# Performance work log

Hardware: AMD Instinct MI355X
Metric: run time of the kernel (lower is better)

Reference implementation:

```python
import jax, jax.numpy as jnp
import numpy as np

N = 8192          # number of samples (atoms)
D_IN = 256        # in_features (descriptor dim)
D_OUT = 256       # out_features
NUM_TYPE = 64     # number of atom types
INIT_VAL = 0.01


def setup_inputs() -> dict:
    key = jax.random.key(0)
    k1, k2, k3, k4 = jax.random.split(key, 4)
    batch_i = jax.random.randint(k1, (N,), 0, NUM_TYPE)                     # [N] type index per sample
    batch_descriptor = jax.random.normal(k2, (N, D_IN), dtype=jnp.float32)  # [N, D_IN]
    layer1 = INIT_VAL * jax.random.normal(k3, (NUM_TYPE, D_OUT, D_IN), dtype=jnp.float32)
    W = INIT_VAL * jax.random.normal(k4, (D_OUT, D_IN), dtype=jnp.float32)  # linear_adjust.weight
    b = jnp.zeros((D_OUT,), dtype=jnp.float32)                              # linear_adjust.bias (init 0)
    return {"batch_i": batch_i, "batch_descriptor": batch_descriptor,
            "layer1": layer1, "W": W, "b": b}


def reference(batch_i, batch_descriptor, layer1, W, b):
    # Per-sample type-indexed weight gather + batched mat-vec (torch.bmm)
    # layer1[batch_i]: [N, D_OUT, D_IN]; descriptor: [N, D_IN] -> [N, D_OUT]
    gathered = layer1[batch_i]
    out = jnp.einsum('noi,ni->no', gathered, batch_descriptor)
    out = jnp.tanh(out)  # ACT assumed tanh (undefined in snippet)
    # linear_adjust: x @ W.T + b
    adjust = batch_descriptor @ W.T + b
    return out + adjust
```

## Files before the change

kernel.cpp:

```cpp
#include <hip/hip_runtime.h>
#include <cstddef>

#define NUM_TYPE 64
#define DD 256
#define NN 8192
#define GM64 192
#define PSTR 264

typedef __bf16 bf16x8 __attribute__((ext_vector_type(8)));
typedef __bf16 bf16x4 __attribute__((ext_vector_type(4)));
typedef float f32x4 __attribute__((ext_vector_type(4)));

__device__ __forceinline__ bf16x4 cvt4(float4 v) {
  bf16x4 h;
  h[0] = (__bf16)v.x; h[1] = (__bf16)v.y; h[2] = (__bf16)v.z; h[3] = (__bf16)v.w;
  return h;
}

__device__ __forceinline__ float tanh_fast(float x) {
  float xc = fminf(fmaxf(x, -15.f), 15.f);
  float e = __expf(2.f * xc);
  return (e - 1.f) / (e + 1.f);
}

__global__ __launch_bounds__(1024) void perm_conv(
    const int* __restrict__ bi,
    const float* __restrict__ desc,
    const float* __restrict__ W,
    int* __restrict__ type_off, int* __restrict__ perm,
    int* __restrict__ gtype, int* __restrict__ gfirst,
    __bf16* __restrict__ descB, __bf16* __restrict__ Wb) {
  const int b = blockIdx.x;
  const int tid = threadIdx.x;
  if (b == 0) {
    __shared__ int wcnt[16][NUM_TYPE];
    __shared__ int wbase[16][NUM_TYPE];
    __shared__ int cnt[NUM_TYPE];
    __shared__ int tstart[NUM_TYPE];
    __shared__ int gbase[NUM_TYPE];
    __shared__ int totals[2];
    const int w = tid >> 6;
    for (int i = tid; i < 16 * NUM_TYPE; i += 1024) ((int*)wcnt)[i] = 0;
    __syncthreads();
    int myv[8];
#pragma unroll
    for (int rnd = 0; rnd < 8; ++rnd) {
      int v = bi[rnd * 1024 + tid];
      myv[rnd] = v;
      atomicAdd(&wcnt[w][v], 1);
    }
    __syncthreads();
    if (tid < NUM_TYPE) {
      int s = 0;
#pragma unroll
      for (int ww = 0; ww < 16; ++ww) { wbase[ww][tid] = s; s += wcnt[ww][tid]; }
      cnt[tid] = s;
    }
    __syncthreads();
    if (tid == 0) {
      int s = 0, p = 0;
      for (int t = 0; t < NUM_TYPE; ++t) {
        tstart[t] = s; gbase[t] = p;
        s += cnt[t];
        p += (cnt[t] + 63) >> 6;
      }
      totals[0] = s; totals[1] = p;
    }
    __syncthreads();
    if (tid < NUM_TYPE) {
      const int c = cnt[tid];
      const int ngr = (c + 63) >> 6;
      const int g0 = gbase[tid];
      const int s0 = tstart[tid];
      for (int j = 0; j < ngr; ++j) { gtype[g0 + j] = tid; gfirst[g0 + j] = s0 + j * 64; }
      type_off[tid] = s0;
#pragma unroll
      for (int ww = 0; ww < 16; ++ww) wbase[ww][tid] += s0;
    }
    if (tid == 0) type_off[NUM_TYPE] = totals[0];
    for (int g = totals[1] + tid; g < GM64; g += 1024) gtype[g] = -1;
    __syncthreads();
#pragma unroll
    for (int rnd = 0; rnd < 8; ++rnd) {
      int v = myv[rnd];
      int p = atomicAdd(&wbase[w][v], 1);
      perm[p] = rnd * 1024 + tid;
    }
  } else {
    const float4* srcD = reinterpret_cast<const float4*>(desc);
    const float4* srcW = reinterpret_cast<const float4*>(W);
#pragma unroll
    for (int it = 0; it < 4; ++it) {
      const int idx = (b - 1) * 4096 + it * 1024 + tid;
      if (idx < 524288)
        *reinterpret_cast<bf16x4*>(descB + (size_t)idx * 4) = cvt4(srcD[idx]);
      else
        *reinterpret_cast<bf16x4*>(Wb + (size_t)(idx - 524288) * 4) = cvt4(srcW[idx - 524288]);
    }
  }
}

__global__ __launch_bounds__(1024, 1) void gemm_resident(
    const __bf16* __restrict__ descB,
    const float* __restrict__ layer1,
    const __bf16* __restrict__ Wb,
    const float* __restrict__ bias,
    const int* __restrict__ type_off,
    const int* __restrict__ perm,
    float* __restrict__ out) {
  extern __shared__ __bf16 lds[];
  __bf16* At = lds;
  __bf16* Ll = lds + 64 * PSTR;
  __bf16* Wl = lds + 2 * 64 * PSTR;

  const int bid = blockIdx.x;
  const int t = bid >> 2;
  const int cb = bid & 3;
  const int off = type_off[t];
  const int limit = type_off[t + 1];
  const int cnt = limit - off;
  if (cnt <= 0) return;
  const int ngr = (cnt + 63) >> 6;

  const int tid = threadIdx.x;
  const int wid = tid >> 6;
  const int lane = tid & 63;
  const int l15 = lane & 15;
  const int lg = lane >> 4;
  const int wr = wid & 3;
  const int wc = wid >> 2;

  {
    const float* Lsrc = layer1 + ((size_t)t * DD + cb * 64) * DD;
#pragma unroll
    for (int it = 0; it < 4; ++it) {
      const int idx = it * 1024 + tid;
      const int col = idx >> 6, seg = idx & 63;
      float4 v = *reinterpret_cast<const float4*>(Lsrc + (size_t)col * DD + seg * 4);
      *reinterpret_cast<bf16x4*>(Ll + col * PSTR + seg * 4) = cvt4(v);
    }
    const __bf16* Wsrc = Wb + (size_t)cb * 64 * DD;
#pragma unroll
    for (int it = 0; it < 2; ++it) {
      const int idx = it * 1024 + tid;
      const int col = idx >> 5, seg = idx & 31;
      *reinterpret_cast<bf16x8*>(Wl + col * PSTR + seg * 8) =
          *reinterpret_cast<const bf16x8*>(Wsrc + (size_t)col * DD + seg * 8);
    }
  }

  const int colg = cb * 64 + wc * 16 + l15;
  const float bv = bias[colg];

  for (int j = 0; j < ngr; ++j) {
    const int first = off + j * 64;
#pragma unroll
    for (int it = 0; it < 2; ++it) {
      const int idx = it * 1024 + tid;
      const int row = idx >> 5, seg = idx & 31;
      const int rr = first + row;
      const int s = (rr < limit) ? perm[rr] : -1;
      bf16x8 v = {};
      if (s >= 0) v = *reinterpret_cast<const bf16x8*>(descB + (size_t)s * DD + seg * 8);
      *reinterpret_cast<bf16x8*>(At + row * PSTR + seg * 8) = v;
    }
    __syncthreads();

    f32x4 accL = {0.f, 0.f, 0.f, 0.f};
    f32x4 accW = {0.f, 0.f, 0.f, 0.f};
#pragma unroll
    for (int kc = 0; kc < 8; ++kc) {
      bf16x8 af = *reinterpret_cast<const bf16x8*>(At + (wr * 16 + l15) * PSTR + kc * 32 + lg * 8);
      bf16x8 bl = *reinterpret_cast<const bf16x8*>(Ll + (wc * 16 + l15) * PSTR + kc * 32 + lg * 8);
      bf16x8 bw = *reinterpret_cast<const bf16x8*>(Wl + (wc * 16 + l15) * PSTR + kc * 32 + lg * 8);
      accL = __builtin_amdgcn_mfma_f32_16x16x32_bf16(af, bl, accL, 0, 0, 0);
      accW = __builtin_amdgcn_mfma_f32_16x16x32_bf16(af, bw, accW, 0, 0, 0);
    }

    const int orow = first + wr * 16 + l15;
    const int sOut = (orow < limit) ? perm[orow] : -1;
#pragma unroll
    for (int i = 0; i < 4; ++i) {
      const int sv = __shfl(sOut, lg * 4 + i, 64);
      if (sv >= 0)
        __builtin_nontemporal_store(tanh_fast(accL[i]) + accW[i] + bv,
                                    out + (size_t)sv * DD + colg);
    }
    __syncthreads();
  }
}

extern "C" void kernel_launch(void* const* d_in, const int* in_sizes, int n_in,
                              void* d_out, int out_size, void* d_ws, size_t ws_size,
                              hipStream_t stream) {
  const int* bi       = (const int*)d_in[0];
  const float* desc   = (const float*)d_in[1];
  const float* layer1 = (const float*)d_in[2];
  const float* W      = (const float*)d_in[3];
  const float* bias   = (const float*)d_in[4];
  float* out = (float*)d_out;

  char* ws = (char*)d_ws;
  int* type_off = (int*)(ws);
  int* gtype    = (int*)(ws + 1024);
  int* gfirst   = (int*)(ws + 4096);
  int* perm     = (int*)(ws + 8192);
  __bf16* descB = (__bf16*)(ws + 65536);
  __bf16* Wb    = (__bf16*)(ws + 65536 + 4194304);

  const int ldsBytes = 3 * 64 * PSTR * 2;

  hipLaunchKernelGGL(perm_conv, dim3(133), dim3(1024), 0, stream,
                     bi, desc, W, type_off, perm, gtype, gfirst, descB, Wb);
  hipLaunchKernelGGL(gemm_resident, dim3(256), dim3(1024), ldsBytes, stream,
                     descB, layer1, Wb, bias, type_off, perm, out);
}
```

Before: 29.08 us.

## Fuse type bucketing and bf16 conversion into single per-type GEMM kernel

Removes the separate permutation/conversion kernel. Each block now scans the full type-index array itself, builds its own row list for its type in LDS with a wave prefix scan, and converts the fp32 descriptor and W to bf16 on load inside the GEMM. This drops one kernel launch and the global round trip of the bf16 copies and the permutation array. In exchange, every block redundantly reads all 8192 type indices, and the descriptor gather now reads fp32 rather than bf16.

Result: slower. 52.11 us (+79.2%).

```diff
diff --git a/kernel.cpp b/kernel.cpp
--- a/kernel.cpp
+++ b/kernel.cpp
@@ -4,7 +4,6 @@
 #define NUM_TYPE 64
 #define DD 256
 #define NN 8192
-#define GM64 192
 #define PSTR 264
 
 typedef __bf16 bf16x8 __attribute__((ext_vector_type(8)));
@@ -23,146 +22,92 @@
   return (e - 1.f) / (e + 1.f);
 }
 
-__global__ __launch_bounds__(1024) void perm_conv(
+__global__ __launch_bounds__(1024, 1) void fused_all(
     const int* __restrict__ bi,
     const float* __restrict__ desc,
+    const float* __restrict__ layer1,
     const float* __restrict__ W,
-    int* __restrict__ type_off, int* __restrict__ perm,
-    int* __restrict__ gtype, int* __restrict__ gfirst,
-    __bf16* __restrict__ descB, __bf16* __restrict__ Wb) {
-  const int b = blockIdx.x;
-  const int tid = threadIdx.x;
-  if (b == 0) {
-    __shared__ int wcnt[16][NUM_TYPE];
-    __shared__ int wbase[16][NUM_TYPE];
-    __shared__ int cnt[NUM_TYPE];
-    __shared__ int tstart[NUM_TYPE];
-    __shared__ int gbase[NUM_TYPE];
-    __shared__ int totals[2];
-    const int w = tid >> 6;
-    for (int i = tid; i < 16 * NUM_TYPE; i += 1024) ((int*)wcnt)[i] = 0;
-    __syncthreads();
-    int myv[8];
-#pragma unroll
-    for (int rnd = 0; rnd < 8; ++rnd) {
-      int v = bi[rnd * 1024 + tid];
-      myv[rnd] = v;
-      atomicAdd(&wcnt[w][v], 1);
-    }
-    __syncthreads();
-    if (tid < NUM_TYPE) {
-      int s = 0;
-#pragma unroll
-      for (int ww = 0; ww < 16; ++ww) { wbase[ww][tid] = s; s += wcnt[ww][tid]; }
-      cnt[tid] = s;
-    }
-    __syncthreads();
-    if (tid == 0) {
-      int s = 0, p = 0;
-      for (int t = 0; t < NUM_TYPE; ++t) {
-        tstart[t] = s; gbase[t] = p;
-        s += cnt[t];
-        p += (cnt[t] + 63) >> 6;
-      }
-      totals[0] = s; totals[1] = p;
-    }
-    __syncthreads();
-    if (tid < NUM_TYPE) {
-      const int c = cnt[tid];
-      const int ngr = (c + 63) >> 6;
-      const int g0 = gbase[tid];
-      const int s0 = tstart[tid];
-      for (int j = 0; j < ngr; ++j) { gtype[g0 + j] = tid; gfirst[g0 + j] = s0 + j * 64; }
-      type_off[tid] = s0;
-#pragma unroll
-      for (int ww = 0; ww < 16; ++ww) wbase[ww][tid] += s0;
-    }
-    if (tid == 0) type_off[NUM_TYPE] = totals[0];
-    for (int g = totals[1] + tid; g < GM64; g += 1024) gtype[g] = -1;
-    __syncthreads();
-#pragma unroll
-    for (int rnd = 0; rnd < 8; ++rnd) {
-      int v = myv[rnd];
-      int p = atomicAdd(&wbase[w][v], 1);
-      perm[p] = rnd * 1024 + tid;
-    }
-  } else {
-    const float4* srcD = reinterpret_cast<const float4*>(desc);
-    const float4* srcW = reinterpret_cast<const float4*>(W);
-#pragma unroll
-    for (int it = 0; it < 4; ++it) {
-      const int idx = (b - 1) * 4096 + it * 1024 + tid;
-      if (idx < 524288)
-        *reinterpret_cast<bf16x4*>(descB + (size_t)idx * 4) = cvt4(srcD[idx]);
-      else
-        *reinterpret_cast<bf16x4*>(Wb + (size_t)(idx - 524288) * 4) = cvt4(srcW[idx - 524288]);
-    }
-  }
-}
-
-__global__ __launch_bounds__(1024, 1) void gemm_resident(
-    const __bf16* __restrict__ descB,
-    const float* __restrict__ layer1,
-    const __bf16* __restrict__ Wb,
     const float* __restrict__ bias,
-    const int* __restrict__ type_off,
-    const int* __restrict__ perm,
     float* __restrict__ out) {
-  extern __shared__ __bf16 lds[];
-  __bf16* At = lds;
-  __bf16* Ll = lds + 64 * PSTR;
-  __bf16* Wl = lds + 2 * 64 * PSTR;
+  extern __shared__ char smem[];
+  __bf16* At = (__bf16*)smem;
+  __bf16* Ll = At + 64 * PSTR;
+  __bf16* Wl = Ll + 64 * PSTR;
+  int* rlist = (int*)(Wl + 64 * PSTR);
+  __shared__ int scanbuf[16];
+  __shared__ int totcnt;
 
   const int bid = blockIdx.x;
   const int t = bid >> 2;
   const int cb = bid & 3;
-  const int off = type_off[t];
-  const int limit = type_off[t + 1];
-  const int cnt = limit - off;
-  if (cnt <= 0) return;
-  const int ngr = (cnt + 63) >> 6;
+  const int tid = threadIdx.x;
+  const int lane = tid & 63;
+  const int wid = tid >> 6;
 
-  const int tid = threadIdx.x;
-  const int wid = tid >> 6;
-  const int lane = tid & 63;
+  int flags = 0, c = 0;
+  const int ebase = tid * 8;
+#pragma unroll
+  for (int k = 0; k < 8; ++k) {
+    const int m = (bi[ebase + k] == t) ? 1 : 0;
+    flags |= m << k;
+    c += m;
+  }
+  int sc = c;
+#pragma unroll
+  for (int d = 1; d < 64; d <<= 1) {
+    const int o = __shfl_up(sc, d, 64);
+    if (lane >= d) sc += o;
+  }
+  if (lane == 63) scanbuf[wid] = sc;
+  __syncthreads();
+  if (tid == 0) {
+    int s = 0;
+#pragma unroll
+    for (int i = 0; i < 16; ++i) { const int v = scanbuf[i]; scanbuf[i] = s; s += v; }
+    totcnt = s;
+  }
+  __syncthreads();
+  int pos = scanbuf[wid] + sc - c;
+#pragma unroll
+  for (int k = 0; k < 8; ++k)
+    if (flags & (1 << k)) rlist[pos++] = ebase + k;
+  const int cnt = totcnt;
+  __syncthreads();
+  if (cnt == 0) return;
+
+  {
+    const float* Lsrc = layer1 + ((size_t)t * DD + cb * 64) * DD;
+    const float* Wsrc = W + (size_t)(cb * 64) * DD;
+#pragma unroll
+    for (int it = 0; it < 4; ++it) {
+      const int idx = it * 1024 + tid;
+      const int col = idx >> 6, seg = idx & 63;
+      *reinterpret_cast<bf16x4*>(Ll + col * PSTR + seg * 4) =
+          cvt4(*reinterpret_cast<const float4*>(Lsrc + (size_t)col * DD + seg * 4));
+      *reinterpret_cast<bf16x4*>(Wl + col * PSTR + seg * 4) =
+          cvt4(*reinterpret_cast<const float4*>(Wsrc + (size_t)col * DD + seg * 4));
+    }
+  }
+
   const int l15 = lane & 15;
   const int lg = lane >> 4;
   const int wr = wid & 3;
   const int wc = wid >> 2;
+  const int colg = cb * 64 + wc * 16 + l15;
+  const float bv = bias[colg];
+  const int ngr = (cnt + 63) >> 6;
 
-  {
-    const float* Lsrc = layer1 + ((size_t)t * DD + cb * 64) * DD;
+  for (int j = 0; j < ngr; ++j) {
+    const int first = j * 64;
+    __syncthreads();
 #pragma unroll
     for (int it = 0; it < 4; ++it) {
       const int idx = it * 1024 + tid;
-      const int col = idx >> 6, seg = idx & 63;
-      float4 v = *reinterpret_cast<const float4*>(Lsrc + (size_t)col * DD + seg * 4);
-      *reinterpret_cast<bf16x4*>(Ll + col * PSTR + seg * 4) = cvt4(v);
-    }
-    const __bf16* Wsrc = Wb + (size_t)cb * 64 * DD;
-#pragma unroll
-    for (int it = 0; it < 2; ++it) {
-      const int idx = it * 1024 + tid;
-      const int col = idx >> 5, seg = idx & 31;
-      *reinterpret_cast<bf16x8*>(Wl + col * PSTR + seg * 8) =
-          *reinterpret_cast<const bf16x8*>(Wsrc + (size_t)col * DD + seg * 8);
-    }
-  }
-
-  const int colg = cb * 64 + wc * 16 + l15;
-  const float bv = bias[colg];
-
-  for (int j = 0; j < ngr; ++j) {
-    const int first = off + j * 64;
-#pragma unroll
-    for (int it = 0; it < 2; ++it) {
-      const int idx = it * 1024 + tid;
-      const int row = idx >> 5, seg = idx & 31;
+      const int row = idx >> 6, seg = idx & 63;
       const int rr = first + row;
-      const int s = (rr < limit) ? perm[rr] : -1;
-      bf16x8 v = {};
-      if (s >= 0) v = *reinterpret_cast<const bf16x8*>(descB + (size_t)s * DD + seg * 8);
-      *reinterpret_cast<bf16x8*>(At + row * PSTR + seg * 8) = v;
+      float4 v = make_float4(0.f, 0.f, 0.f, 0.f);
+      if (rr < cnt) v = *reinterpret_cast<const float4*>(desc + (size_t)rlist[rr] * DD + seg * 4);
+      *reinterpret_cast<bf16x4*>(At + row * PSTR + seg * 4) = cvt4(v);
     }
     __syncthreads();
 
@@ -178,7 +123,7 @@
     }
 
     const int orow = first + wr * 16 + l15;
-    const int sOut = (orow < limit) ? perm[orow] : -1;
+    const int sOut = (orow < cnt) ? rlist[orow] : -1;
 #pragma unroll
     for (int i = 0; i < 4; ++i) {
       const int sv = __shfl(sOut, lg * 4 + i, 64);
@@ -186,7 +131,6 @@
         __builtin_nontemporal_store(tanh_fast(accL[i]) + accW[i] + bv,
                                     out + (size_t)sv * DD + colg);
     }
-    __syncthreads();
   }
 }
 
@@ -200,18 +144,8 @@
   const float* bias   = (const float*)d_in[4];
   float* out = (float*)d_out;
 
-  char* ws = (char*)d_ws;
-  int* type_off = (int*)(ws);
-  int* gtype    = (int*)(ws + 1024);
-  int* gfirst   = (int*)(ws + 4096);
-  int* perm     = (int*)(ws + 8192);
-  __bf16* descB = (__bf16*)(ws + 65536);
-  __bf16* Wb    = (__bf16*)(ws + 65536 + 4194304);
+  const int ldsBytes = 3 * 64 * PSTR * 2 + NN * 4;
 
-  const int ldsBytes = 3 * 64 * PSTR * 2;
-
-  hipLaunchKernelGGL(perm_conv, dim3(133), dim3(1024), 0, stream,
-                     bi, desc, W, type_off, perm, gtype, gfirst, descB, Wb);
-  hipLaunchKernelGGL(gemm_resident, dim3(256), dim3(1024), ldsBytes, stream,
-                     descB, layer1, Wb, bias, type_off, perm, out);
+  hipLaunchKernelGGL(fused_all, dim3(256), dim3(1024), ldsBytes, stream,
+                     bi, desc, layer1, W, bias, out);
 }
```

## Split GEMM into 32-column blocks of 512 threads with type-interleaved grid

Applied to the files above, without the earlier changes.

The resident GEMM now uses 512 blocks of 512 threads, each covering 32 output columns instead of 64. The block index is remapped so neighbouring blocks handle different types, and two blocks can share a CU. The conversion kernel uses twice as many blocks, each doing half the work, and the unused group-table outputs are removed. The barrier moves to the top of the row-group loop. The aim is more parallelism and better load balance across CUs, at the cost of loading the A tile twice per type.

Measured after the change: 25.65 us. -11.8%, faster.

```diff
diff --git a/kernel.cpp b/kernel.cpp
--- a/kernel.cpp
+++ b/kernel.cpp
@@ -28,7 +28,6 @@
     const float* __restrict__ desc,
     const float* __restrict__ W,
     int* __restrict__ type_off, int* __restrict__ perm,
-    int* __restrict__ gtype, int* __restrict__ gfirst,
     __bf16* __restrict__ descB, __bf16* __restrict__ Wb) {
   const int b = blockIdx.x;
   const int tid = threadIdx.x;
@@ -37,8 +36,7 @@
     __shared__ int wbase[16][NUM_TYPE];
     __shared__ int cnt[NUM_TYPE];
     __shared__ int tstart[NUM_TYPE];
-    __shared__ int gbase[NUM_TYPE];
-    __shared__ int totals[2];
+    __shared__ int totals[1];
     const int w = tid >> 6;
     for (int i = tid; i < 16 * NUM_TYPE; i += 1024) ((int*)wcnt)[i] = 0;
     __syncthreads();
@@ -58,27 +56,18 @@
     }
     __syncthreads();
     if (tid == 0) {
-      int s = 0, p = 0;
-      for (int t = 0; t < NUM_TYPE; ++t) {
-        tstart[t] = s; gbase[t] = p;
-        s += cnt[t];
-        p += (cnt[t] + 63) >> 6;
-      }
-      totals[0] = s; totals[1] = p;
+      int s = 0;
+      for (int t = 0; t < NUM_TYPE; ++t) { tstart[t] = s; s += cnt[t]; }
+      totals[0] = s;
     }
     __syncthreads();
     if (tid < NUM_TYPE) {
-      const int c = cnt[tid];
-      const int ngr = (c + 63) >> 6;
-      const int g0 = gbase[tid];
       const int s0 = tstart[tid];
-      for (int j = 0; j < ngr; ++j) { gtype[g0 + j] = tid; gfirst[g0 + j] = s0 + j * 64; }
       type_off[tid] = s0;
 #pragma unroll
       for (int ww = 0; ww < 16; ++ww) wbase[ww][tid] += s0;
     }
     if (tid == 0) type_off[NUM_TYPE] = totals[0];
-    for (int g = totals[1] + tid; g < GM64; g += 1024) gtype[g] = -1;
     __syncthreads();
 #pragma unroll
     for (int rnd = 0; rnd < 8; ++rnd) {
@@ -90,8 +79,8 @@
     const float4* srcD = reinterpret_cast<const float4*>(desc);
     const float4* srcW = reinterpret_cast<const float4*>(W);
 #pragma unroll
-    for (int it = 0; it < 4; ++it) {
-      const int idx = (b - 1) * 4096 + it * 1024 + tid;
+    for (int it = 0; it < 2; ++it) {
+      const int idx = (b - 1) * 2048 + it * 1024 + tid;
       if (idx < 524288)
         *reinterpret_cast<bf16x4*>(descB + (size_t)idx * 4) = cvt4(srcD[idx]);
       else
@@ -100,7 +89,7 @@
   }
 }
 
-__global__ __launch_bounds__(1024, 1) void gemm_resident(
+__global__ __launch_bounds__(512, 2) void gemm_res32(
     const __bf16* __restrict__ descB,
     const float* __restrict__ layer1,
     const __bf16* __restrict__ Wb,
@@ -111,11 +100,11 @@
   extern __shared__ __bf16 lds[];
   __bf16* At = lds;
   __bf16* Ll = lds + 64 * PSTR;
-  __bf16* Wl = lds + 2 * 64 * PSTR;
-
-  const int bid = blockIdx.x;
-  const int t = bid >> 2;
-  const int cb = bid & 3;
+  __bf16* Wl = lds + 96 * PSTR;
+
+  const int d = blockIdx.x;
+  const int t = (d & 7) + 8 * ((d >> 3) & 7);
+  const int cb = d >> 6;
   const int off = type_off[t];
   const int limit = type_off[t + 1];
   const int cnt = limit - off;
@@ -127,41 +116,41 @@
   const int lane = tid & 63;
   const int l15 = lane & 15;
   const int lg = lane >> 4;
-  const int wr = wid & 3;
-  const int wc = wid >> 2;
+  const int wr = wid >> 1;
+  const int wc = wid & 1;
 
   {
-    const float* Lsrc = layer1 + ((size_t)t * DD + cb * 64) * DD;
+    const float* Lsrc = layer1 + ((size_t)t * DD + cb * 32) * DD;
 #pragma unroll
     for (int it = 0; it < 4; ++it) {
-      const int idx = it * 1024 + tid;
+      const int idx = it * 512 + tid;
       const int col = idx >> 6, seg = idx & 63;
-      float4 v = *reinterpret_cast<const float4*>(Lsrc + (size_t)col * DD + seg * 4);
-      *reinterpret_cast<bf16x4*>(Ll + col * PSTR + seg * 4) = cvt4(v);
-    }
-    const __bf16* Wsrc = Wb + (size_t)cb * 64 * DD;
+      *reinterpret_cast<bf16x4*>(Ll + col * PSTR + seg * 4) =
+          cvt4(*reinterpret_cast<const float4*>(Lsrc + (size_t)col * DD + seg * 4));
+    }
+    const __bf16* Wsrc = Wb + (size_t)(cb * 32) * DD;
 #pragma unroll
     for (int it = 0; it < 2; ++it) {
-      const int idx = it * 1024 + tid;
+      const int idx = it * 512 + tid;
       const int col = idx >> 5, seg = idx & 31;
       *reinterpret_cast<bf16x8*>(Wl + col * PSTR + seg * 8) =
           *reinterpret_cast<const bf16x8*>(Wsrc + (size_t)col * DD + seg * 8);
     }
   }
 
-  const int colg = cb * 64 + wc * 16 + l15;
+  const int colg = cb * 32 + wc * 16 + l15;
   const float bv = bias[colg];
 
   for (int j = 0; j < ngr; ++j) {
     const int first = off + j * 64;
-#pragma unroll
-    for (int it = 0; it < 2; ++it) {
-      const int idx = it * 1024 + tid;
+    if (j > 0) __syncthreads();
+#pragma unroll
+    for (int it = 0; it < 4; ++it) {
+      const int idx = it * 512 + tid;
       const int row = idx >> 5, seg = idx & 31;
       const int rr = first + row;
-      const int s = (rr < limit) ? perm[rr] : -1;
       bf16x8 v = {};
-      if (s >= 0) v = *reinterpret_cast<const bf16x8*>(descB + (size_t)s * DD + seg * 8);
+      if (rr < limit) v = *reinterpret_cast<const bf16x8*>(descB + (size_t)perm[rr] * DD + seg * 8);
       *reinterpret_cast<bf16x8*>(At + row * PSTR + seg * 8) = v;
     }
     __syncthreads();
@@ -186,7 +175,6 @@
         __builtin_nontemporal_store(tanh_fast(accL[i]) + accW[i] + bv,
                                     out + (size_t)sv * DD + colg);
     }
-    __syncthreads();
   }
 }
 
@@ -202,16 +190,14 @@
 
   char* ws = (char*)d_ws;
   int* type_off = (int*)(ws);
-  int* gtype    = (int*)(ws + 1024);
-  int* gfirst   = (int*)(ws + 4096);
   int* perm     = (int*)(ws + 8192);
   __bf16* descB = (__bf16*)(ws + 65536);
   __bf16* Wb    = (__bf16*)(ws + 65536 + 4194304);
 
-  const int ldsBytes = 3 * 64 * PSTR * 2;
-
-  hipLaunchKernelGGL(perm_conv, dim3(133), dim3(1024), 0, stream,
-                     bi, desc, W, type_off, perm, gtype, gfirst, descB, Wb);
-  hipLaunchKernelGGL(gemm_resident, dim3(256), dim3(1024), ldsBytes, stream,
+  const int ldsBytes = 128 * PSTR * 2;
+
+  hipLaunchKernelGGL(perm_conv, dim3(265), dim3(1024), 0, stream,
+                     bi, desc, W, type_off, perm, descB, Wb);
+  hipLaunchKernelGGL(gemm_res32, dim3(512), dim3(512), ldsBytes, stream,
                      descB, layer1, Wb, bias, type_off, perm, out);
 }
```
